# Optimization experiments

Measured on AMD Instinct MI355X. Metric: run time of the kernel, lower is better.

Reference implementation:

```python
import jax, jax.numpy as jnp
import numpy as np

F1, F2, F3 = 128, 64, 32
K = 16          # tensor_neurons
BINS = 16
FEAT = K + BINS # feature_count with histogram
BN1, BN2, BN3 = 16, 8, 4
NLAB = 128


def gcn(x, W, b, src, dst, n):
    # PyG GCNConv: h = x W; symmetric norm with self-loops; aggregate at dst.
    h = x @ W
    deg = jax.ops.segment_sum(jnp.ones(src.shape[0], h.dtype), dst, num_segments=n) + 1.0
    dinv = deg ** -0.5
    norm = (dinv[src] * dinv[dst])[:, None]
    agg = jax.ops.segment_sum(h[src] * norm, dst, num_segments=n)
    return agg + h * (dinv ** 2)[:, None] + b  # second term = self-loop


def conv_pass(feat, ei, w1, b1, w2, b2, w3, b3):
    n = feat.shape[0]
    src, dst = ei[0], ei[1]
    h = jax.nn.relu(gcn(feat, w1, b1, src, dst, n))
    h = jax.nn.relu(gcn(h, w2, b2, src, dst, n))
    return gcn(h, w3, b3, src, dst, n)  # [n, F3]


def att_pool(x, W):
    ctx = jnp.tanh(jnp.mean(x @ W, axis=0))      # [F3]
    sig = jax.nn.sigmoid(x @ ctx)                # [n]
    return x.T @ sig                             # [F3]


def histc_norm(a, b):
    # torch.histc with bins over [min, max] of the (detached) scores.
    s = jax.lax.stop_gradient(a @ b.T).reshape(-1)  # [N1*N2]
    lo, hi = s.min(), s.max()
    idx = jnp.clip(jnp.floor((s - lo) / jnp.maximum(hi - lo, 1e-12) * BINS).astype(jnp.int32), 0, BINS - 1)
    h = jax.ops.segment_sum(jnp.ones_like(s), idx, num_segments=BINS)
    return h / h.sum()


def setup_inputs() -> dict:
    key = jax.random.key(0)
    ks = jax.random.split(key, 24)
    N, E = 20000, 640000
    d = {
        'features_1': jax.random.normal(ks[0], (N, NLAB), jnp.float32),
        'features_2': jax.random.normal(ks[1], (N, NLAB), jnp.float32),
        'edge_index_1': jax.random.randint(ks[2], (2, E), 0, N),
        'edge_index_2': jax.random.randint(ks[3], (2, E), 0, N),
        'avg_v': jax.random.uniform(ks[4], (1,), jnp.float32) * 10.0 + 5.0,
    }
    def w(k, shape, fan_in):
        return jax.random.normal(k, shape, jnp.float32) * (1.0 / np.sqrt(fan_in))
    d['w1'] = w(ks[5], (NLAB, F1), NLAB); d['b1'] = jnp.zeros((F1,), jnp.float32)
    d['w2'] = w(ks[6], (F1, F2), F1);     d['b2'] = jnp.zeros((F2,), jnp.float32)
    d['w3'] = w(ks[7], (F2, F3), F2);     d['b3'] = jnp.zeros((F3,), jnp.float32)
    d['attn_w'] = w(ks[8], (F3, F3), F3)
    d['ntn_w'] = w(ks[9], (F3, F3, K), F3)
    d['ntn_v'] = w(ks[10], (K, 2 * F3), 2 * F3)
    d['ntn_b'] = jnp.zeros((K,), jnp.float32)
    d['fc1_w'] = w(ks[11], (FEAT, BN1), FEAT); d['fc1_b'] = jnp.zeros((BN1,), jnp.float32)
    d['fc2_w'] = w(ks[12], (BN1, BN2), BN1);   d['fc2_b'] = jnp.zeros((BN2,), jnp.float32)
    d['fc3_w'] = w(ks[13], (BN2, BN3), BN2);   d['fc3_b'] = jnp.zeros((BN3,), jnp.float32)
    d['score_w'] = w(ks[14], (BN3, 1), BN3);   d['score_b'] = jnp.zeros((1,), jnp.float32)
    return d


def reference(features_1, features_2, avg_v,
              w1, b1, w2, b2, w3, b3,
              attn_w, ntn_w, ntn_v, ntn_b,
              fc1_w, fc1_b, fc2_w, fc2_b, fc3_w, fc3_b,
              score_w, score_b,
              edge_index_1, edge_index_2):
    a1 = conv_pass(features_1, edge_index_1, w1, b1, w2, b2, w3, b3)  # [N1, F3]
    a2 = conv_pass(features_2, edge_index_2, w1, b1, w2, b2, w3, b3)  # [N2, F3]
    p1 = att_pool(a1, attn_w)  # [F3]
    p2 = att_pool(a2, attn_w)  # [F3]
    ntn = jax.nn.relu(jnp.einsum('i,ijk,j->k', p1, ntn_w, p2)
                      + ntn_v @ jnp.concatenate([p1, p2]) + ntn_b)  # [K]
    hist = histc_norm(a1, a2)  # [BINS]
    s = jnp.concatenate([ntn, hist])[None, :]  # [1, FEAT]
    s = jax.nn.relu(s @ fc1_w + fc1_b)
    s = jax.nn.relu(s @ fc2_w + fc2_b)
    s = jax.nn.relu(s @ fc3_w + fc3_b)
    score = jax.nn.sigmoid((s @ score_w + score_b).reshape(-1))  # [1]
    pre_ged = -jnp.log(score) * avg_v  # target_mode == 'exp'
    return score, pre_ged
```

## Files before the change

kernel.cpp:

```cpp
#include <hip/hip_runtime.h>


typedef short s16x8 __attribute__((ext_vector_type(8)));
typedef float f32x4 __attribute__((ext_vector_type(4)));


__global__ __launch_bounds__(256) void count_kern(const int* __restrict__ ei1,
                                                  const int* __restrict__ ei2,
                                                  int* counts, int N, int E)
{
    int g = blockIdx.y;
    const int* dst = (g ? ei2 : ei1) + E;
    int* cnt = counts + (size_t)g * N;
    for (int e = blockIdx.x * 256 + threadIdx.x; e < E; e += gridDim.x * 256)
        atomicAdd(&cnt[dst[e]], 1);
}

__global__ __launch_bounds__(256) void dinv_kern(const int* __restrict__ counts,
                                                 float* dinv, int N)
{
    int g = blockIdx.y;
    int i = blockIdx.x * 256 + threadIdx.x;
    if (i < N) dinv[(size_t)g * N + i] = 1.0f / sqrtf((float)counts[(size_t)g * N + i] + 1.0f);
}

__global__ __launch_bounds__(1024) void scan_kern(const int* __restrict__ counts,
                                                  int* row_ptr, int* cursor, int N)
{
    int g = blockIdx.x;
    const int* cnt = counts + (size_t)g * N;
    int* rp  = row_ptr + (size_t)g * (N + 1);
    int* cur = cursor  + (size_t)g * (N + 1);
    __shared__ int lds[1024];
    int t = threadIdx.x;
    int CH = (N + 1023) >> 10;
    int base = t * CH;
    int sum = 0;
    for (int i = 0; i < CH; i++) {
        int idx = base + i;
        if (idx < N) sum += cnt[idx];
    }
    lds[t] = sum;
    __syncthreads();
    for (int s = 1; s < 1024; s <<= 1) {
        int add = (t >= s) ? lds[t - s] : 0;
        __syncthreads();
        lds[t] += add;
        __syncthreads();
    }
    int run = lds[t] - sum;
    if (t == 0) rp[0] = 0;
    for (int i = 0; i < CH; i++) {
        int idx = base + i;
        if (idx < N) {
            int v = cnt[idx];
            cur[idx] = run;
            run += v;
            rp[idx + 1] = run;
        }
    }
}

__global__ __launch_bounds__(256) void scatter_kern(const int* __restrict__ ei1,
                                                    const int* __restrict__ ei2,
                                                    int* cursor, int* col, int N, int E)
{
    int g = blockIdx.y;
    const int* ei = g ? ei2 : ei1;
    const int* src = ei;
    const int* dst = ei + E;
    int* cur = cursor + (size_t)g * (N + 1);
    int* cl  = col    + (size_t)g * E;
    int e = blockIdx.x * 256 + threadIdx.x;
    if (e < E) {
        int pos = atomicAdd(&cur[dst[e]], 1);
        cl[pos] = src[e];
    }
}


template <int K, int NCOL>
__global__ __launch_bounds__(256) void gemm_kern(const float* __restrict__ xa,
                                                 const float* __restrict__ xb,
                                                 const float* __restrict__ W,
                                                 const float* __restrict__ dinva,
                                                 const float* __restrict__ dinvb,
                                                 float* ya, float* yb, int nodes)
{
    int g = blockIdx.y;
    const float* x = g ? xb : xa;
    const float* dinv = g ? dinvb : dinva;
    float* y = g ? yb : ya;
    constexpr int MB  = 32;
    constexpr int NG  = 256 / NCOL;
    constexpr int RPT = MB / NG;
    __shared__ float xs[MB][K];
    int row0 = blockIdx.x * MB;
    int t = threadIdx.x;
    constexpr int TOT = MB * K / 4;
    for (int i = t; i < TOT; i += 256) {
        int lin = i * 4;
        int r = lin / K, k = lin % K;
        float4 v = make_float4(0.f, 0.f, 0.f, 0.f);
        if (row0 + r < nodes) v = *(const float4*)&x[(size_t)(row0 + r) * K + k];
        *(float4*)&xs[r][k] = v;
    }
    __syncthreads();
    int c  = t % NCOL;
    int rg = t / NCOL;
    float acc[RPT];
#pragma unroll
    for (int i = 0; i < RPT; i++) acc[i] = 0.f;
    for (int k = 0; k < K; k++) {
        float w = W[k * NCOL + c];
#pragma unroll
        for (int i = 0; i < RPT; i++) acc[i] += xs[rg * RPT + i][k] * w;
    }
#pragma unroll
    for (int i = 0; i < RPT; i++) {
        int r = row0 + rg * RPT + i;
        if (r < nodes) y[(size_t)r * NCOL + c] = acc[i] * dinv[r];
    }
}


template <int F, bool RELU>
__global__ __launch_bounds__(256) void agg_kern(const float* __restrict__ ha,
                                                const float* __restrict__ hb,
                                                const int* __restrict__ colA,
                                                const int* __restrict__ colB,
                                                const int* __restrict__ rpA,
                                                const int* __restrict__ rpB,
                                                const float* __restrict__ dinvA,
                                                const float* __restrict__ dinvB,
                                                const float* __restrict__ bias,
                                                float* ya, float* yb, int nodes)
{
    int g = blockIdx.y;
    const float4* hp  = (const float4*)(g ? hb : ha);
    const int*   col  = g ? colB : colA;
    const int*   rp   = g ? rpB : rpA;
    const float* dinv = g ? dinvB : dinvA;
    float4* y = (float4*)(g ? yb : ya);
    constexpr int TPN = F / 4;
    constexpr int NPB = 256 / TPN;
    int t = threadIdx.x;
    int ni = blockIdx.x * NPB + t / TPN;
    int f4 = t % TPN;
    if (ni >= nodes) return;
    int e0 = rp[ni], e1 = rp[ni + 1];
    float ax = 0.f, ay = 0.f, az = 0.f, aw = 0.f;
    int e = e0;
    for (; e + 4 <= e1; e += 4) {
        int c0 = col[e], c1 = col[e + 1], c2 = col[e + 2], c3 = col[e + 3];
        float4 v0 = hp[(size_t)c0 * TPN + f4];
        float4 v1 = hp[(size_t)c1 * TPN + f4];
        float4 v2 = hp[(size_t)c2 * TPN + f4];
        float4 v3 = hp[(size_t)c3 * TPN + f4];
        ax += (v0.x + v1.x) + (v2.x + v3.x);
        ay += (v0.y + v1.y) + (v2.y + v3.y);
        az += (v0.z + v1.z) + (v2.z + v3.z);
        aw += (v0.w + v1.w) + (v2.w + v3.w);
    }
    for (; e < e1; e++) {
        float4 v = hp[(size_t)col[e] * TPN + f4];
        ax += v.x; ay += v.y; az += v.z; aw += v.w;
    }
    float4 self = hp[(size_t)ni * TPN + f4];
    float di = dinv[ni];
    float4 bv = ((const float4*)bias)[f4];
    float ox = di * (ax + self.x) + bv.x;
    float oy = di * (ay + self.y) + bv.y;
    float oz = di * (az + self.z) + bv.z;
    float ow = di * (aw + self.w) + bv.w;
    if (RELU) {
        ox = fmaxf(ox, 0.f); oy = fmaxf(oy, 0.f);
        oz = fmaxf(oz, 0.f); ow = fmaxf(ow, 0.f);
    }
    y[(size_t)ni * TPN + f4] = make_float4(ox, oy, oz, ow);
}


__global__ __launch_bounds__(256) void colsum_kern(const float* __restrict__ a1,
                                                   const float* __restrict__ a2,
                                                   float* colsum, int nodes)
{
    int g = blockIdx.y;
    const float* a = g ? a2 : a1;
    float* cs = colsum + g * 32;
    int t = threadIdx.x;
    int c = t & 31, rr = t >> 5;
    float acc = 0.f;
    for (int r = blockIdx.x * 8 + rr; r < nodes; r += gridDim.x * 8)
        acc += a[(size_t)r * 32 + c];
    __shared__ float lds[256];
    lds[t] = acc;
    __syncthreads();
    if (t < 32) {
        float s = 0.f;
#pragma unroll
        for (int j = 0; j < 8; j++) s += lds[j * 32 + t];
        atomicAdd(&cs[t], s);
    }
}

__global__ void ctx_kern(const float* __restrict__ colsum, const float* __restrict__ W,
                         float* ctx, float invN)
{
    int g = blockIdx.x;
    const float* cs = colsum + g * 32;
    int c = threadIdx.x;
    float s = 0.f;
    for (int j = 0; j < 32; j++) s += cs[j] * invN * W[j * 32 + c];
    ctx[g * 32 + c] = tanhf(s);
}

__global__ __launch_bounds__(256) void pool_kern(const float* __restrict__ a1,
                                                 const float* __restrict__ a2,
                                                 const float* __restrict__ ctx,
                                                 float* pooled, int nodes)
{
    int g = blockIdx.y;
    const float* a  = g ? a2 : a1;
    const float* cx = ctx + g * 32;
    float* pl = pooled + g * 32;
    int t = threadIdx.x;
    int c = t & 31, rr = t >> 5;
    float cxc = cx[c];
    float acc = 0.f;
    for (int r = blockIdx.x * 8 + rr; r < nodes; r += gridDim.x * 8) {
        float v = a[(size_t)r * 32 + c];
        float d = v * cxc;
#pragma unroll
        for (int m = 16; m >= 1; m >>= 1) d += __shfl_xor(d, m, 32);
        acc += v * (1.f / (1.f + expf(-d)));
    }
    __shared__ float lds[256];
    lds[t] = acc;
    __syncthreads();
    if (t < 32) {
        float s = 0.f;
#pragma unroll
        for (int j = 0; j < 8; j++) s += lds[j * 32 + t];
        atomicAdd(&pl[t], s);
    }
}


__global__ __launch_bounds__(512) void ntn_kern(const float* __restrict__ pooled,
                                                const float* __restrict__ ntn_w,
                                                const float* __restrict__ ntn_v,
                                                const float* __restrict__ ntn_b,
                                                float* ntn)
{
    const float* p1 = pooled;
    const float* p2 = pooled + 32;
    __shared__ float lds[512];
    int t = threadIdx.x;
    int i = t >> 4, k = t & 15;
    float s = 0.f;
    for (int j = 0; j < 32; j++) s += ntn_w[(i * 32 + j) * 16 + k] * p2[j];
    lds[t] = s * p1[i];
    __syncthreads();
    if (t < 16) {
        float v = 0.f;
        for (int ii = 0; ii < 32; ii++) v += lds[ii * 16 + t];
        for (int j = 0; j < 32; j++) v += ntn_v[t * 64 + j] * p1[j];
        for (int j = 0; j < 32; j++) v += ntn_v[t * 64 + 32 + j] * p2[j];
        v += ntn_b[t];
        ntn[t] = fmaxf(v, 0.f);
    }
}


__device__ __forceinline__ unsigned encf(float f)
{
    unsigned b = __float_as_uint(f);
    return b ^ (unsigned)(((int)b >> 31) | 0x80000000);
}
__device__ __forceinline__ float decf(unsigned u)
{
    unsigned b = (u & 0x80000000u) ? (u ^ 0x80000000u) : ~u;
    return __uint_as_float(b);
}

__device__ __forceinline__ unsigned short f2bf(float f)
{
    unsigned u = __float_as_uint(f);
    return (unsigned short)((u + 0x7FFFu + ((u >> 16) & 1u)) >> 16);
}

template <int SCALED>
__global__ __launch_bounds__(256) void split_kern(const float* __restrict__ a,
                                                  const float* __restrict__ prep,
                                                  unsigned short* __restrict__ hi,
                                                  unsigned short* __restrict__ lo,
                                                  int total4)
{
    int i = blockIdx.x * 256 + threadIdx.x;
    if (i >= total4) return;
    float4 v = ((const float4*)a)[i];
    if (SCALED) {
        float sc = prep[1];
        v.x *= sc; v.y *= sc; v.z *= sc; v.w *= sc;
    }
    ushort4 h, l;
    h.x = f2bf(v.x); l.x = f2bf(v.x - __uint_as_float((unsigned)h.x << 16));
    h.y = f2bf(v.y); l.y = f2bf(v.y - __uint_as_float((unsigned)h.y << 16));
    h.z = f2bf(v.z); l.z = f2bf(v.z - __uint_as_float((unsigned)h.z << 16));
    h.w = f2bf(v.w); l.w = f2bf(v.w - __uint_as_float((unsigned)h.w << 16));
    ((ushort4*)hi)[i] = h;
    ((ushort4*)lo)[i] = l;
}

__global__ void prep_kern(const unsigned* __restrict__ encMinArr,
                          const unsigned* __restrict__ encMaxArr,
                          float* __restrict__ prep)
{
    __shared__ unsigned ru[4], rv[4];
    int t = threadIdx.x;
    unsigned mnu = encMinArr[t];
    unsigned mxu = encMaxArr[t];
#pragma unroll
    for (int m = 32; m >= 1; m >>= 1) {
        unsigned a = (unsigned)__shfl_xor((int)mnu, m);
        unsigned b = (unsigned)__shfl_xor((int)mxu, m);
        mnu = a < mnu ? a : mnu;
        mxu = b > mxu ? b : mxu;
    }
    if ((t & 63) == 0) { ru[t >> 6] = mnu; rv[t >> 6] = mxu; }
    __syncthreads();
    if (t == 0) {
        mnu = ru[0]; mxu = rv[0];
#pragma unroll
        for (int j = 1; j < 4; j++) {
            mnu = ru[j] < mnu ? ru[j] : mnu;
            mxu = rv[j] > mxu ? rv[j] : mxu;
        }
        float lo = decf(mnu), hi = decf(mxu);
        float scale = 16.f / fmaxf(hi - lo, 1e-12f);
        prep[0] = lo;
        prep[1] = scale;
        prep[2] = -lo * scale;
    }
}

__device__ __forceinline__ s16x8 ldfrag(const unsigned short* __restrict__ base,
                                        int node0, int lane)
{
    const unsigned short* p = base + (size_t)(node0 + (lane & 15)) * 32 + 8 * (lane >> 4);
    return *(const s16x8*)p;
}

template <int PASS>
__global__ __launch_bounds__(256) void hist_pass(const unsigned short* __restrict__ h1,
                                                 const unsigned short* __restrict__ l1,
                                                 const unsigned short* __restrict__ h2,
                                                 const unsigned short* __restrict__ l2,
                                                 const float* __restrict__ prep,
                                                 unsigned* encMinArr, unsigned* encMaxArr,
                                                 unsigned* histSub)
{
    int t = threadIdx.x, w = t >> 6, lane = t & 63;
    int row0 = blockIdx.x * 160 + (w >> 1) * 80;
    int col0 = blockIdx.y * 160 + (w & 1) * 80;
    __shared__ unsigned wh[(PASS == 1) ? 4 : 1][16][64];
    __shared__ float rf[4], rg[4];

    float nls = 0.f;
    if (PASS == 1) {
        for (int i = t; i < 4096; i += 256) ((unsigned*)wh)[i] = 0u;
        nls = prep[2];
        __syncthreads();
    }
    f32x4 cinit = {nls, nls, nls, nls};

    s16x8 ah[5], al[5];
#pragma unroll
    for (int r = 0; r < 5; r++) {
        ah[r] = ldfrag(h1, row0 + r * 16, lane);
        al[r] = ldfrag(l1, row0 + r * 16, lane);
    }
    float mn = 3.4e38f, mx = -3.4e38f;
#pragma unroll
    for (int c = 0; c < 5; c++) {
        s16x8 bh = ldfrag(h2, col0 + c * 16, lane);
        s16x8 bl = ldfrag(l2, col0 + c * 16, lane);
        f32x4 acc[5];
#pragma unroll
        for (int r = 0; r < 5; r++) {
            f32x4 z = cinit;
            z = __builtin_amdgcn_mfma_f32_16x16x32_bf16(ah[r], bh, z, 0, 0, 0);
            z = __builtin_amdgcn_mfma_f32_16x16x32_bf16(al[r], bh, z, 0, 0, 0);
            z = __builtin_amdgcn_mfma_f32_16x16x32_bf16(ah[r], bl, z, 0, 0, 0);
            acc[r] = z;
        }
#pragma unroll
        for (int r = 0; r < 5; r++)
#pragma unroll
            for (int j = 0; j < 4; j++) {
                float s = acc[r][j];
                if (PASS == 0) {
                    mn = fminf(mn, s);
                    mx = fmaxf(mx, s);
                } else {
                    int bi = (int)fminf(fmaxf(s, 0.f), 15.f);
                    atomicAdd(&wh[w][bi][lane], 1u);
                }
            }
    }

    int slot = (int)((blockIdx.x * gridDim.y + blockIdx.y) & 255u);
    if (PASS == 0) {
#pragma unroll
        for (int m = 32; m >= 1; m >>= 1) {
            mn = fminf(mn, __shfl_xor(mn, m));
            mx = fmaxf(mx, __shfl_xor(mx, m));
        }
        if (lane == 0) { rf[w] = mn; rg[w] = mx; }
        __syncthreads();
        if (t == 0) {
            mn = fminf(fminf(rf[0], rf[1]), fminf(rf[2], rf[3]));
            mx = fmaxf(fmaxf(rg[0], rg[1]), fmaxf(rg[2], rg[3]));
            atomicMin(&encMinArr[slot], encf(mn));
            atomicMax(&encMaxArr[slot], encf(mx));
        }
    } else {
        __syncthreads();
        for (int s = 32; s > 0; s >>= 1) {
            for (int idx = t; idx < 4 * 16 * s; idx += 256) {
                int ww  = idx / (16 * s);
                int rem = idx - ww * 16 * s;
                int b   = rem / s;
                int l2i = rem - b * s;
                wh[ww][b][l2i] += wh[ww][b][l2i + s];
            }
            __syncthreads();
        }
        if (t < 16) {
            unsigned tot = wh[0][t][0] + wh[1][t][0] + wh[2][t][0] + wh[3][t][0];
            if (tot) atomicAdd(&histSub[slot * 16 + t], tot);
        }
    }
}


__global__ __launch_bounds__(256) void final_kern(const float* __restrict__ ntn,
                           const unsigned* __restrict__ histSub,
                           const float* __restrict__ fc1w, const float* __restrict__ fc1b,
                           const float* __restrict__ fc2w, const float* __restrict__ fc2b,
                           const float* __restrict__ fc3w, const float* __restrict__ fc3b,
                           const float* __restrict__ scw, const float* __restrict__ scb,
                           const float* __restrict__ avg_v, float* out)
{
    __shared__ unsigned part[256];
    __shared__ float s_fc1w[512];
    __shared__ float s_fc2w[128];
    __shared__ float s_fc3w[32];
    __shared__ float s_fc1b[16], s_fc2b[8], s_fc3b[4], s_scw[4];
    __shared__ float s_feat[32];
    __shared__ float s_h1[16], s_h2[8], s_h3[4];
    __shared__ float s_scb, s_avg, s_inv;
    int t = threadIdx.x;

    s_fc1w[t]       = fc1w[t];
    s_fc1w[t + 256] = fc1w[t + 256];
    if (t < 128)               s_fc2w[t] = fc2w[t];
    else if (t < 160)          s_fc3w[t - 128] = fc3w[t - 128];
    else if (t < 176)          s_fc1b[t - 160] = fc1b[t - 160];
    else if (t < 184)          s_fc2b[t - 176] = fc2b[t - 176];
    else if (t < 188)          s_fc3b[t - 184] = fc3b[t - 184];
    else if (t < 192)          s_scw[t - 188]  = scw[t - 188];
    else if (t < 208)          s_feat[t - 192] = ntn[t - 192];
    else if (t == 208)         s_scb = scb[0];
    else if (t == 209)         s_avg = avg_v[0];

    int b = t & 15, grp = t >> 4;
    unsigned s = 0;
    for (int i = grp; i < 256; i += 16) s += histSub[i * 16 + b];
    part[t] = s;
    __syncthreads();
    if (t < 16) {
        unsigned tot = 0;
#pragma unroll
        for (int j = 0; j < 16; j++) tot += part[j * 16 + t];
        part[t] = tot;
    }
    __syncthreads();
    if (t == 0) {
        float total = 0.f;
#pragma unroll
        for (int j = 0; j < 16; j++) total += (float)part[j];
        s_inv = 1.f / total;
    }
    __syncthreads();
    if (t < 16) s_feat[16 + t] = (float)part[t] * s_inv;
    __syncthreads();

    if (t < 16) {
        float s2 = s_fc1b[t];
#pragma unroll
        for (int i = 0; i < 32; i++) s2 += s_feat[i] * s_fc1w[i * 16 + t];
        s_h1[t] = fmaxf(s2, 0.f);
    }
    __syncthreads();
    if (t < 8) {
        float s2 = s_fc2b[t];
#pragma unroll
        for (int i = 0; i < 16; i++) s2 += s_h1[i] * s_fc2w[i * 8 + t];
        s_h2[t] = fmaxf(s2, 0.f);
    }
    __syncthreads();
    if (t < 4) {
        float s2 = s_fc3b[t];
#pragma unroll
        for (int i = 0; i < 8; i++) s2 += s_h2[i] * s_fc3w[i * 4 + t];
        s_h3[t] = fmaxf(s2, 0.f);
    }
    __syncthreads();
    if (t == 0) {
        float sc = s_scb;
#pragma unroll
        for (int i = 0; i < 4; i++) sc += s_h3[i] * s_scw[i];
        float score = 1.f / (1.f + expf(-sc));
        out[0] = score;
        out[1] = -logf(fmaxf(score, 1e-37f)) * s_avg;
    }
}


extern "C" void kernel_launch(void* const* d_in, const int* in_sizes, int n_in,
                              void* d_out, int out_size, void* d_ws, size_t ws_size,
                              hipStream_t stream)
{
    (void)n_in; (void)out_size; (void)ws_size;
    const float* feat1 = (const float*)d_in[0];
    const float* feat2 = (const float*)d_in[1];
    const int*   ei1   = (const int*)d_in[2];
    const int*   ei2   = (const int*)d_in[3];
    const float* avg_v = (const float*)d_in[4];
    const float* w1 = (const float*)d_in[5];
    const float* b1 = (const float*)d_in[6];
    const float* w2 = (const float*)d_in[7];
    const float* b2 = (const float*)d_in[8];
    const float* w3 = (const float*)d_in[9];
    const float* b3 = (const float*)d_in[10];
    const float* attn_w = (const float*)d_in[11];
    const float* ntn_w  = (const float*)d_in[12];
    const float* ntn_v  = (const float*)d_in[13];
    const float* ntn_b  = (const float*)d_in[14];
    const float* fc1w = (const float*)d_in[15];
    const float* fc1b = (const float*)d_in[16];
    const float* fc2w = (const float*)d_in[17];
    const float* fc2b = (const float*)d_in[18];
    const float* fc3w = (const float*)d_in[19];
    const float* fc3b = (const float*)d_in[20];
    const float* scw  = (const float*)d_in[21];
    const float* scb  = (const float*)d_in[22];

    const int N = in_sizes[0] / 128;
    const int E = in_sizes[2] / 2;

    char* ws = (char*)d_ws;
    size_t o = 0;
    auto take = [&](size_t bytes) -> void* {
        void* p = ws + o;
        o += (bytes + 255) & ~(size_t)255;
        return p;
    };
    size_t zbeg = o;
    int*      counts    = (int*)     take((size_t)2 * N * 4);
    float*    zero0     = (float*)   take(128 * 4);
    unsigned* histSub   = (unsigned*)take(256 * 16 * 4);
    unsigned* encMaxArr = (unsigned*)take(256 * 4);
    size_t zend = o;
    unsigned* encMinArr = (unsigned*)take(256 * 4);
    int*   rp   = (int*)  take((size_t)2 * (N + 1) * 4);
    int*   cur  = (int*)  take((size_t)2 * (N + 1) * 4);
    float* dinv = (float*)take((size_t)2 * N * 4);
    int*   col  = (int*)  take((size_t)2 * E * 4);
    float* bufA = (float*)take((size_t)2 * N * 128 * 4);
    float* bufB = (float*)take((size_t)2 * N * 128 * 4);
    float* aout = (float*)take((size_t)2 * N * 32 * 4);
    float* ctx  = (float*)take(64 * 4);
    float* ntn  = (float*)take(16 * 4);
    float* prep = (float*)take(4 * 4);
    float* colsum = zero0;
    float* pooled = zero0 + 64;
    unsigned short* hiP  = (unsigned short*)bufA;
    unsigned short* loP  = hiP + (size_t)2 * N * 32;
    unsigned short* hiS  = (unsigned short*)bufB;
    unsigned short* loS  = hiS + (size_t)2 * N * 32;

    hipMemsetAsync(ws + zbeg, 0, zend - zbeg, stream);
    hipMemsetAsync(encMinArr, 0xFF, 256 * 4, stream);

    count_kern<<<dim3(512, 2), 256, 0, stream>>>(ei1, ei2, counts, N, E);
    dinv_kern<<<dim3((N + 255) / 256, 2), 256, 0, stream>>>(counts, dinv, N);
    scan_kern<<<2, 1024, 0, stream>>>(counts, rp, cur, N);
    scatter_kern<<<dim3((E + 255) / 256, 2), 256, 0, stream>>>(ei1, ei2, cur, col, N, E);

    float* bufA2 = bufA + (size_t)N * 128;
    float* bufB2 = bufB + (size_t)N * 128;
    float* a2p   = aout + (size_t)N * 32;
    const int* col2 = col + (size_t)E;
    const int* rp2  = rp + (N + 1);
    const float* dinv2 = dinv + N;

    gemm_kern<128, 128><<<dim3((N + 31) / 32, 2), 256, 0, stream>>>(feat1, feat2, w1, dinv, dinv2, bufB, bufB2, N);
    agg_kern<128, true><<<dim3((N + 7) / 8, 2), 256, 0, stream>>>(bufB, bufB2, col, col2, rp, rp2, dinv, dinv2, b1, bufA, bufA2, N);
    gemm_kern<128, 64><<<dim3((N + 31) / 32, 2), 256, 0, stream>>>(bufA, bufA2, w2, dinv, dinv2, bufB, bufB2, N);
    agg_kern<64, true><<<dim3((N + 15) / 16, 2), 256, 0, stream>>>(bufB, bufB2, col, col2, rp, rp2, dinv, dinv2, b2, bufA, bufA2, N);
    gemm_kern<64, 32><<<dim3((N + 31) / 32, 2), 256, 0, stream>>>(bufA, bufA2, w3, dinv, dinv2, bufB, bufB2, N);
    agg_kern<32, false><<<dim3((N + 31) / 32, 2), 256, 0, stream>>>(bufB, bufB2, col, col2, rp, rp2, dinv, dinv2, b3, aout, a2p, N);

    colsum_kern<<<dim3(64, 2), 256, 0, stream>>>(aout, a2p, colsum, N);
    ctx_kern<<<2, 32, 0, stream>>>(colsum, attn_w, ctx, 1.f / (float)N);
    pool_kern<<<dim3(64, 2), 256, 0, stream>>>(aout, a2p, ctx, pooled, N);

    ntn_kern<<<1, 512, 0, stream>>>(pooled, ntn_w, ntn_v, ntn_b, ntn);

    int tot4 = 2 * N * 32 / 4;
    split_kern<0><<<(tot4 + 255) / 256, 256, 0, stream>>>(aout, prep, hiP, loP, tot4);
    unsigned short* hiP2 = hiP + (size_t)N * 32;
    unsigned short* loP2 = loP + (size_t)N * 32;
    unsigned short* hiS2 = hiS + (size_t)N * 32;
    unsigned short* loS2 = loS + (size_t)N * 32;
    dim3 hgrid(N / 160, N / 160);
    hist_pass<0><<<hgrid, 256, 0, stream>>>(hiP, loP, hiP2, loP2, prep, encMinArr, encMaxArr, histSub);
    prep_kern<<<1, 256, 0, stream>>>(encMinArr, encMaxArr, prep);
    split_kern<1><<<(tot4 + 255) / 256, 256, 0, stream>>>(aout, prep, hiS, loS, tot4);
    hist_pass<1><<<hgrid, 256, 0, stream>>>(hiS, loS, hiS2, loS2, prep, encMinArr, encMaxArr, histSub);

    final_kern<<<1, 256, 0, stream>>>(ntn, histSub, fc1w, fc1b, fc2w, fc2b, fc3w, fc3b,
                                      scw, scb, avg_v, (float*)d_out);
}
```

Before: 728.3 us.

## Drop hi/lo split in min/max pass, reuse unscaled a2 split, cheapen bin index

The min/max pass now uses only the bf16 high parts (one MFMA instead of three), so its scores are less precise. In the binning pass only a1 is pre-scaled and split; the already-split unscaled a2 is reused, which removes half the second split work. The bin index now comes from a single float-to-unsigned conversion of a 4096-scaled score, masked into a byte offset for the shared-memory atomic. The risk is that approximate min/max values from the high-only pass could shift the bin edges, and clamping now depends on the scale factor and the mask bits.

Result: faster. 691.8 us (-5.0%).

```diff
diff --git a/kernel.cpp b/kernel.cpp
--- a/kernel.cpp
+++ b/kernel.cpp
@@ -338,10 +338,10 @@
             mxu = rv[j] > mxu ? rv[j] : mxu;
         }
         float lo = decf(mnu), hi = decf(mxu);
-        float scale = 16.f / fmaxf(hi - lo, 1e-12f);
+        float scaleA = 4096.f * (1.f - 1e-4f) / fmaxf(hi - lo, 1e-12f);
         prep[0] = lo;
-        prep[1] = scale;
-        prep[2] = -lo * scale;
+        prep[1] = scaleA;
+        prep[2] = -lo * scaleA;
     }
 }
 
@@ -368,9 +368,11 @@
     __shared__ float rf[4], rg[4];
 
     float nls = 0.f;
+    unsigned laneoff = 0;
     if (PASS == 1) {
         for (int i = t; i < 4096; i += 256) ((unsigned*)wh)[i] = 0u;
         nls = prep[2];
+        laneoff = ((unsigned)w << 12) | ((unsigned)lane << 2);
         __syncthreads();
     }
     f32x4 cinit = {nls, nls, nls, nls};
@@ -379,20 +381,23 @@
 #pragma unroll
     for (int r = 0; r < 5; r++) {
         ah[r] = ldfrag(h1, row0 + r * 16, lane);
-        al[r] = ldfrag(l1, row0 + r * 16, lane);
+        if (PASS == 1) al[r] = ldfrag(l1, row0 + r * 16, lane);
     }
     float mn = 3.4e38f, mx = -3.4e38f;
 #pragma unroll
     for (int c = 0; c < 5; c++) {
         s16x8 bh = ldfrag(h2, col0 + c * 16, lane);
-        s16x8 bl = ldfrag(l2, col0 + c * 16, lane);
+        s16x8 bl;
+        if (PASS == 1) bl = ldfrag(l2, col0 + c * 16, lane);
         f32x4 acc[5];
 #pragma unroll
         for (int r = 0; r < 5; r++) {
             f32x4 z = cinit;
             z = __builtin_amdgcn_mfma_f32_16x16x32_bf16(ah[r], bh, z, 0, 0, 0);
-            z = __builtin_amdgcn_mfma_f32_16x16x32_bf16(al[r], bh, z, 0, 0, 0);
-            z = __builtin_amdgcn_mfma_f32_16x16x32_bf16(ah[r], bl, z, 0, 0, 0);
+            if (PASS == 1) {
+                z = __builtin_amdgcn_mfma_f32_16x16x32_bf16(al[r], bh, z, 0, 0, 0);
+                z = __builtin_amdgcn_mfma_f32_16x16x32_bf16(ah[r], bl, z, 0, 0, 0);
+            }
             acc[r] = z;
         }
 #pragma unroll
@@ -404,8 +409,10 @@
                     mn = fminf(mn, s);
                     mx = fmaxf(mx, s);
                 } else {
-                    int bi = (int)fminf(fmaxf(s, 0.f), 15.f);
-                    atomicAdd(&wh[w][bi][lane], 1u);
+                    unsigned u;
+                    asm("v_cvt_u32_f32_e32 %0, %1" : "=v"(u) : "v"(s));
+                    unsigned idx = (u & 0xF00u) | laneoff;
+                    atomicAdd((unsigned*)((char*)wh + idx), 1u);
                 }
             }
     }
@@ -590,7 +597,7 @@
     unsigned short* hiP  = (unsigned short*)bufA;
     unsigned short* loP  = hiP + (size_t)2 * N * 32;
     unsigned short* hiS  = (unsigned short*)bufB;
-    unsigned short* loS  = hiS + (size_t)2 * N * 32;
+    unsigned short* loS  = hiS + (size_t)N * 32;
 
     hipMemsetAsync(ws + zbeg, 0, zend - zbeg, stream);
     hipMemsetAsync(encMinArr, 0xFF, 256 * 4, stream);
@@ -620,17 +627,16 @@
 
     ntn_kern<<<1, 512, 0, stream>>>(pooled, ntn_w, ntn_v, ntn_b, ntn);
 
-    int tot4 = 2 * N * 32 / 4;
-    split_kern<0><<<(tot4 + 255) / 256, 256, 0, stream>>>(aout, prep, hiP, loP, tot4);
+    int tot4all = 2 * N * 32 / 4;
+    int tot4a   = N * 32 / 4;
+    split_kern<0><<<(tot4all + 255) / 256, 256, 0, stream>>>(aout, prep, hiP, loP, tot4all);
     unsigned short* hiP2 = hiP + (size_t)N * 32;
     unsigned short* loP2 = loP + (size_t)N * 32;
-    unsigned short* hiS2 = hiS + (size_t)N * 32;
-    unsigned short* loS2 = loS + (size_t)N * 32;
     dim3 hgrid(N / 160, N / 160);
     hist_pass<0><<<hgrid, 256, 0, stream>>>(hiP, loP, hiP2, loP2, prep, encMinArr, encMaxArr, histSub);
     prep_kern<<<1, 256, 0, stream>>>(encMinArr, encMaxArr, prep);
-    split_kern<1><<<(tot4 + 255) / 256, 256, 0, stream>>>(aout, prep, hiS, loS, tot4);
-    hist_pass<1><<<hgrid, 256, 0, stream>>>(hiS, loS, hiS2, loS2, prep, encMinArr, encMaxArr, histSub);
+    split_kern<1><<<(tot4a + 255) / 256, 256, 0, stream>>>(aout, prep, hiS, loS, tot4a);
+    hist_pass<1><<<hgrid, 256, 0, stream>>>(hiS, loS, hiP2, loP2, prep, encMinArr, encMaxArr, histSub);
 
     final_kern<<<1, 256, 0, stream>>>(ntn, histSub, fc1w, fc1b, fc2w, fc2b, fc3w, fc3b,
                                       scw, scb, avg_v, (float*)d_out);
```
